# Kernel optimization log

Hardware: AMD Instinct MI355X
Metric: run time of the kernel (lower is better)

The kernel has to match this reference:

```python
import jax, jax.numpy as jnp
import numpy as np

B, S, E, H, FFN, NQ, DEPTH = 2, 2048, 1024, 16, 4096, 4, 2
DK = E // H
LN_EPS = 1e-5


def _layernorm(t, g, b):
    m = t.mean(-1, keepdims=True)
    v = ((t - m) ** 2).mean(-1, keepdims=True)
    return (t - m) / jnp.sqrt(v + LN_EPS) * g + b


def setup_inputs() -> dict:
    key = jax.random.key(0)
    ks = jax.random.split(key, 12)
    n = lambda i, shape, sc=1.0: (jax.random.normal(ks[i], shape, jnp.float32) * sc)
    return {
        "x": n(0, (B, S, E)),
        "wq": n(1, (E, E), 0.02),
        "wk": n(2, (E, E), 0.02),
        "wv": n(3, (E, E), 0.02),
        "wo": n(4, (E, E), 0.02),
        "w1": n(5, (E, FFN), 0.02),
        "b1": jnp.zeros((FFN,), jnp.float32),
        "w2": n(6, (FFN, E), 0.02),
        "b2": jnp.zeros((E,), jnp.float32),
        "qp_attn": n(7, (NQ, DEPTH)),
        "qp_ffn": n(8, (NQ, DEPTH)),
        "ln1_g": jnp.ones((E,), jnp.float32),
        "ln1_b": jnp.zeros((E,), jnp.float32),
        "ln2_g": jnp.ones((E,), jnp.float32),
        "ln2_b": jnp.zeros((E,), jnp.float32),
    }


def reference(x, wq, wk, wv, wo, w1, b1, w2, b2, qp_attn, qp_ffn,
              ln1_g, ln1_b, ln2_g, ln2_b):
    b, s, _ = x.shape
    # --- quantum attention ---
    q = (x @ wq).reshape(b, s, H, DK)
    k = (x @ wk).reshape(b, s, H, DK)
    v = (x @ wv).reshape(b, s, H, DK)
    scores = jnp.einsum('bqhd,bkhd->bhqk', q, k) / np.sqrt(DK).astype(np.float32)
    attn = jax.nn.softmax(scores, axis=-1)
    classical = jnp.einsum('bhqk,bkhd->bqhd', attn, v)  # (b, s, H, DK)
    # depth-2 RX-only circuit on |0..0>: <Z_0> = cos(sum_d params[0, d]);
    # data-independent scalar broadcast to the first NQ channels of each head
    c_attn = jnp.cos(qp_attn[0].sum())
    mixed = classical.at[..., :NQ].add(c_attn)
    attn_out = mixed.reshape(b, s, E) @ wo
    x1 = _layernorm(x + attn_out, ln1_g, ln1_b)  # dropout is identity in eval
    # --- quantum feed-forward ---
    h = x1 @ w1 + b1  # computed in the source but never consumed by the circuit
    # depth-2 RY-only circuit: <Z_0> = cos(sum_d params[0, d]) -- also data-free
    c_ffn = jnp.cos(qp_ffn[0].sum())
    qvec = jnp.zeros((FFN,), x.dtype).at[:NQ].set(c_ffn)
    ffn_out = jax.nn.relu(qvec) @ w2 + b2  # (E,), broadcast per token
    return _layernorm(x1 + ffn_out, ln2_g, ln2_b)
```

## Files before the change

kernel.cpp:

```cpp
#include <hip/hip_runtime.h>
#include <hip/hip_bf16.h>

typedef unsigned short u16;
using short8 = __attribute__((ext_vector_type(8))) short;
using f32x4  = __attribute__((ext_vector_type(4))) float;
using u32x2  = __attribute__((ext_vector_type(2))) unsigned;

#define S_  2048
#define E_  1024
#define H_  16
#define DK_ 64

#define GLP(p)  ((const __attribute__((address_space(1))) void*)(p))
#define LDSP(p) ((__attribute__((address_space(3))) void*)(p))

__device__ __forceinline__ float b2f(u16 u) {
  union { unsigned int i; float f; } v; v.i = ((unsigned int)u) << 16; return v.f;
}
__device__ __forceinline__ u16 f2b(float f) {
  union { float f; unsigned int i; } v; v.f = f;
  unsigned int r = v.i + 0x7fffu + ((v.i >> 16) & 1u);
  return (u16)(r >> 16);
}
__device__ __forceinline__ unsigned pk2(float a, float b) {
  __hip_bfloat162 h = __float22bfloat162_rn(make_float2(a, b));
  union { __hip_bfloat162 h; unsigned u; } c; c.h = h; return c.u;
}
__device__ __forceinline__ float fexp2(float x) {
#if __has_builtin(__builtin_amdgcn_exp2f)
  return __builtin_amdgcn_exp2f(x);
#else
  return exp2f(x);
#endif
}
__device__ __forceinline__ void plane32_swap(unsigned &dst, unsigned &src) {
#if __has_builtin(__builtin_amdgcn_permlane32_swap)
  u32x2 r = __builtin_amdgcn_permlane32_swap(dst, src, false, false);
  dst = r[0]; src = r[1];
#else
  asm volatile("v_permlane32_swap_b32 %0, %1" : "+v"(dst), "+v"(src));
#endif
}
__device__ __forceinline__ void plane16_swap(unsigned &dst, unsigned &src) {
#if __has_builtin(__builtin_amdgcn_permlane16_swap)
  u32x2 r = __builtin_amdgcn_permlane16_swap(dst, src, false, false);
  dst = r[0]; src = r[1];
#else
  asm volatile("v_permlane16_swap_b32 %0, %1" : "+v"(dst), "+v"(src));
#endif
}

__global__ __launch_bounds__(256) void prep_k(
    const float* __restrict__ x,
    const float* __restrict__ wq, const float* __restrict__ wk,
    const float* __restrict__ wv, const float* __restrict__ wo,
    const float* __restrict__ w2, const float* __restrict__ b2,
    const float* __restrict__ qpf,
    u16* __restrict__ xb, u16* __restrict__ wt, float* __restrict__ fv) {
  __shared__ u16 tile[64][65];
  int id = blockIdx.x, t = threadIdx.x;
  if (id < 2048) {
    size_t i = ((size_t)id * 256 + t) * 8;
    float4 a = *(const float4*)&x[i];
    float4 b = *(const float4*)&x[i + 4];
    uint4 o;
    o.x = pk2(a.x, a.y); o.y = pk2(a.z, a.w);
    o.z = pk2(b.x, b.y); o.w = pk2(b.z, b.w);
    *(uint4*)&xb[i] = o;
  } else if (id < 3072) {
    int i = id - 2048;
    int z = i >> 8; i &= 255;
    const float* src = (z == 0) ? wq : (z == 1) ? wk : (z == 2) ? wv : wo;
    u16* dst = wt + (size_t)z * E_ * E_;
    int k0 = (i & 15) * 64, n0 = (i >> 4) * 64;
    int rr = t >> 4, c4 = (t & 15) * 4;
    for (int p = 0; p < 4; p++) {
      int r = p * 16 + rr;
      float4 v = *(const float4*)&src[(size_t)(k0 + r) * E_ + n0 + c4];
      tile[r][c4] = f2b(v.x); tile[r][c4 + 1] = f2b(v.y);
      tile[r][c4 + 2] = f2b(v.z); tile[r][c4 + 3] = f2b(v.w);
    }
    __syncthreads();
    for (int p = 0; p < 4; p++) {
      int r = p * 16 + rr;
      ushort4 o;
      o.x = tile[c4][r]; o.y = tile[c4 + 1][r]; o.z = tile[c4 + 2][r]; o.w = tile[c4 + 3][r];
      *(ushort4*)&dst[(size_t)(n0 + r) * E_ + k0 + c4] = o;
    }
  } else {
    int e = (id - 3072) * 256 + t;
    float r = fmaxf(cosf(qpf[0] + qpf[1]), 0.f);
    fv[e] = b2[e] + r * (w2[0 * E_ + e] + w2[1 * E_ + e] + w2[2 * E_ + e] + w2[3 * E_ + e]);
  }
}

__device__ __forceinline__ void gemm_loop97(
    const u16* __restrict__ A, const u16* __restrict__ Bt,
    int m0, int n0, f32x4 acc[4][4], u16 (*As)[128][32], u16 (*Bs)[128][32]) {
  int t = threadIdx.x, lane = t & 63, w = t >> 6;
  int wm = w >> 1, wn = w & 1, l15 = lane & 15, quad = lane >> 4;
  int srow = lane >> 2, sch = (lane & 3) * 8;
  const u16 *ga[2], *gb[2];
#pragma unroll
  for (int p = 0; p < 2; p++) {
    int seg = w * 2 + p;
    ga[p] = A + (size_t)(m0 + seg * 16 + srow) * E_ + sch;
    gb[p] = Bt + (size_t)(n0 + seg * 16 + srow) * E_ + sch;
  }
#pragma unroll
  for (int p = 0; p < 2; p++) {
    int seg = w * 2 + p;
    __builtin_amdgcn_global_load_lds(GLP(ga[p]), LDSP(&As[0][seg * 16][0]), 16, 0, 0);
    __builtin_amdgcn_global_load_lds(GLP(gb[p]), LDSP(&Bs[0][seg * 16][0]), 16, 0, 0);
    ga[p] += 32; gb[p] += 32;
  }
  for (int i = 0; i < 32; i++) {
    __syncthreads();
    if (i + 1 < 32) {
      int nb = (i + 1) & 1;
#pragma unroll
      for (int p = 0; p < 2; p++) {
        int seg = w * 2 + p;
        __builtin_amdgcn_global_load_lds(GLP(ga[p]), LDSP(&As[nb][seg * 16][0]), 16, 0, 0);
        __builtin_amdgcn_global_load_lds(GLP(gb[p]), LDSP(&Bs[nb][seg * 16][0]), 16, 0, 0);
        ga[p] += 32; gb[p] += 32;
      }
    }
    int cb = i & 1;
    short8 af[4], bf[4];
#pragma unroll
    for (int ii = 0; ii < 4; ii++) af[ii] = *(const short8*)&As[cb][wm * 64 + ii * 16 + l15][quad * 8];
#pragma unroll
    for (int j = 0; j < 4; j++) bf[j] = *(const short8*)&Bs[cb][wn * 64 + j * 16 + l15][quad * 8];
#pragma unroll
    for (int ii = 0; ii < 4; ii++)
#pragma unroll
      for (int j = 0; j < 4; j++)
        acc[ii][j] = __builtin_amdgcn_mfma_f32_16x16x32_bf16(af[ii], bf[j], acc[ii][j], 0, 0, 0);
  }
}

__global__ __launch_bounds__(256) void qkv_gemm(
    const u16* __restrict__ xb, const u16* __restrict__ wt,
    u16* __restrict__ q, u16* __restrict__ k, u16* __restrict__ vt) {
  __shared__ __align__(16) u16 As[2][128][32];
  __shared__ __align__(16) u16 Bs[2][128][32];
  int bid = blockIdx.x + blockIdx.y * 8;
  int swz = (bid & 7) * 32 + (bid >> 3);
  int n0 = (swz & 7) * 128, m0 = (swz >> 3) * 128, z = blockIdx.z;
  const u16* Bt = wt + (size_t)z * E_ * E_;
  f32x4 acc[4][4];
  f32x4 zero = {0.f, 0.f, 0.f, 0.f};
  for (int i = 0; i < 4; i++)
    for (int j = 0; j < 4; j++) acc[i][j] = zero;
  gemm_loop97(xb, Bt, m0, n0, acc, As, Bs);
  int t = threadIdx.x, lane = t & 63, w = t >> 6;
  int wm = w >> 1, wn = w & 1, l15 = lane & 15, quad = lane >> 4;
  if (z < 2) {
    u16* out = (z == 0) ? q : k;
    float sc = (z == 0) ? 0.18033688f : 1.f;
#pragma unroll
    for (int i = 0; i < 4; i++)
#pragma unroll
      for (int j = 0; j < 4; j++) {
        int mm = m0 + wm * 64 + i * 16 + quad * 4;
        int nn = n0 + wn * 64 + j * 16 + l15;
#pragma unroll
        for (int rr = 0; rr < 4; rr++)
          out[(size_t)(mm + rr) * E_ + nn] = f2b(acc[i][j][rr] * sc);
      }
  } else {
#pragma unroll
    for (int i = 0; i < 4; i++)
#pragma unroll
      for (int j = 0; j < 4; j++) {
        int mm = m0 + wm * 64 + i * 16 + quad * 4;
        int nn = n0 + wn * 64 + j * 16 + l15;
        int b = mm >> 11, s = mm & (S_ - 1);
        size_t base = ((size_t)(b * H_ + (nn >> 6)) * DK_ + (nn & 63)) * S_ + s;
        ushort4 pk;
        pk.x = f2b(acc[i][j][0]); pk.y = f2b(acc[i][j][1]);
        pk.z = f2b(acc[i][j][2]); pk.w = f2b(acc[i][j][3]);
        *(ushort4*)&vt[base] = pk;
      }
  }
}

__global__ __launch_bounds__(256) void oproj_gemm(
    const u16* __restrict__ am, const u16* __restrict__ wot, float* __restrict__ proj) {
  __shared__ __align__(16) u16 As[2][128][32];
  __shared__ __align__(16) u16 Bs[2][128][32];
  int bid = blockIdx.x + blockIdx.y * 8;
  int swz = (bid & 7) * 32 + (bid >> 3);
  int n0 = (swz & 7) * 128, m0 = (swz >> 3) * 128;
  f32x4 acc[4][4];
  f32x4 zero = {0.f, 0.f, 0.f, 0.f};
  for (int i = 0; i < 4; i++)
    for (int j = 0; j < 4; j++) acc[i][j] = zero;
  gemm_loop97(am, wot, m0, n0, acc, As, Bs);
  int t = threadIdx.x, lane = t & 63, w = t >> 6;
  int wm = w >> 1, wn = w & 1, l15 = lane & 15, quad = lane >> 4;
#pragma unroll
  for (int i = 0; i < 4; i++)
#pragma unroll
    for (int j = 0; j < 4; j++) {
      int mm = m0 + wm * 64 + i * 16 + quad * 4;
      int nn = n0 + wn * 64 + j * 16 + l15;
#pragma unroll
      for (int rr = 0; rr < 4; rr++)
        proj[(size_t)(mm + rr) * E_ + nn] = acc[i][j][rr];
    }
}

__global__ __launch_bounds__(256, 4) void attn_kernel(
    const u16* __restrict__ q, const u16* __restrict__ kk,
    const u16* __restrict__ vt, const float* __restrict__ qpa,
    u16* __restrict__ outm) {
  __shared__ __align__(16) u16 KV[2][2][64][64];
  int bid = blockIdx.x + blockIdx.y * 32;
  int swz = (bid & 7) * 128 + (bid >> 3);
  int qt = swz & 31, bh = swz >> 5;
  int b = bh >> 4, h = bh & 15;
  int q0 = qt * 64;
  int t = threadIdx.x, lane = t & 63, w = t >> 6;
  int l15 = lane & 15, quad = lane >> 4;
  int qh = w >> 1, kh = w & 1;
  float c_attn = cosf(qpa[0] + qpa[1]);
  int r8 = lane >> 3, slot = lane & 7;
  size_t kbase = (size_t)(b * S_) * E_ + h * DK_;
  size_t vbase = (size_t)(b * H_ + h) * DK_ * S_;
  const u16 *kptr[2], *vptr[2];
#pragma unroll
  for (int p = 0; p < 2; p++) {
    int row = w * 16 + p * 8 + r8;
    int c = slot ^ (row & 7);
    kptr[p] = kk + kbase + (size_t)row * E_ + c * 8;
    vptr[p] = vt + vbase + (size_t)row * S_ + c * 8;
    __builtin_amdgcn_global_load_lds(GLP(kptr[p]), LDSP(&KV[0][0][w * 16 + p * 8][0]), 16, 0, 0);
    __builtin_amdgcn_global_load_lds(GLP(vptr[p]), LDSP(&KV[0][1][w * 16 + p * 8][0]), 16, 0, 0);
    kptr[p] += (size_t)64 * E_;
    vptr[p] += 64;
  }
  short8 bq[2][2];
#pragma unroll
  for (int nb = 0; nb < 2; nb++) {
    const u16* gq = q + (size_t)(b * S_ + q0 + qh * 32 + nb * 16 + l15) * E_ + h * DK_ + quad * 8;
    bq[nb][0] = *(const short8*)gq;
    bq[nb][1] = *(const short8*)(gq + 32);
  }
  short8 bones;
#pragma unroll
  for (int i = 0; i < 8; i++) bones[i] = (short)0x3F80;
  f32x4 O[2][4], Osum[2];
  f32x4 zero = {0.f, 0.f, 0.f, 0.f};
#pragma unroll
  for (int nb = 0; nb < 2; nb++) {
    Osum[nb] = zero;
#pragma unroll
    for (int j = 0; j < 4; j++) O[nb][j] = zero;
  }
  __syncthreads();
  for (int kt = 0; kt < S_ / 64; kt++) {
    if (kt) __syncthreads();
    if (kt + 1 < S_ / 64) {
      int nb2 = (kt + 1) & 1;
#pragma unroll
      for (int p = 0; p < 2; p++) {
        __builtin_amdgcn_global_load_lds(GLP(kptr[p]), LDSP(&KV[nb2][0][w * 16 + p * 8][0]), 16, 0, 0);
        __builtin_amdgcn_global_load_lds(GLP(vptr[p]), LDSP(&KV[nb2][1][w * 16 + p * 8][0]), 16, 0, 0);
        kptr[p] += (size_t)64 * E_;
        vptr[p] += 64;
      }
    }
    int cb = kt & 1;
    f32x4 sc[2][2];
    __builtin_amdgcn_s_setprio(1);
#pragma unroll
    for (int mb = 0; mb < 2; mb++) {
      int row = kh * 32 + mb * 16 + l15;
      int c0 = quad ^ (row & 7);
      short8 a0 = *(const short8*)&KV[cb][0][row][c0 * 8];
      short8 a1 = *(const short8*)&KV[cb][0][row][(c0 ^ 4) * 8];
#pragma unroll
      for (int nb = 0; nb < 2; nb++) {
        f32x4 z = __builtin_amdgcn_mfma_f32_16x16x32_bf16(a0, bq[nb][0], zero, 0, 0, 0);
        sc[mb][nb] = __builtin_amdgcn_mfma_f32_16x16x32_bf16(a1, bq[nb][1], z, 0, 0, 0);
      }
    }
    __builtin_amdgcn_s_setprio(0);
    short8 bv[4];
#pragma unroll
    for (int nd = 0; nd < 4; nd++) {
      int rv = nd * 16 + l15;
      int cv = (quad | (kh << 2)) ^ (rv & 7);
      bv[nd] = *(const short8*)&KV[cb][1][rv][cv * 8];
    }
    unsigned W[2][2][2];
#pragma unroll
    for (int mb = 0; mb < 2; mb++)
#pragma unroll
      for (int nb = 0; nb < 2; nb++) {
        float p0 = fexp2(sc[mb][nb][0]);
        float p1 = fexp2(sc[mb][nb][1]);
        float p2 = fexp2(sc[mb][nb][2]);
        float p3 = fexp2(sc[mb][nb][3]);
        W[mb][nb][0] = pk2(p0, p1);
        W[mb][nb][1] = pk2(p2, p3);
      }
    union AP { unsigned u[4]; short8 s; };
    AP ap[2];
#pragma unroll
    for (int nb = 0; nb < 2; nb++)
#pragma unroll
      for (int hh = 0; hh < 2; hh++) {
        unsigned a = W[0][nb][hh], bw = W[1][nb][hh];
        plane32_swap(bw, a);
        plane16_swap(a, bw);
        ap[nb].u[hh] = a; ap[nb].u[2 + hh] = bw;
      }
    __builtin_amdgcn_s_setprio(1);
#pragma unroll
    for (int nb = 0; nb < 2; nb++) {
#pragma unroll
      for (int nd = 0; nd < 4; nd++)
        O[nb][nd] = __builtin_amdgcn_mfma_f32_16x16x32_bf16(ap[nb].s, bv[nd], O[nb][nd], 0, 0, 0);
      Osum[nb] = __builtin_amdgcn_mfma_f32_16x16x32_bf16(ap[nb].s, bones, Osum[nb], 0, 0, 0);
    }
    __builtin_amdgcn_s_setprio(0);
  }
  float* red = (float*)KV;
  __syncthreads();
  if (kh) {
    float* dst = red + ((size_t)(qh * 64 + lane)) * 44;
#pragma unroll
    for (int nb = 0; nb < 2; nb++) {
#pragma unroll
      for (int nd = 0; nd < 4; nd++)
        *(f32x4*)&dst[nb * 16 + nd * 4] = O[nb][nd];
      *(f32x4*)&dst[32 + nb * 4] = Osum[nb];
    }
  }
  __syncthreads();
  if (!kh) {
    const float* src = red + ((size_t)(qh * 64 + lane)) * 44;
#pragma unroll
    for (int nb = 0; nb < 2; nb++) {
#pragma unroll
      for (int nd = 0; nd < 4; nd++) {
        f32x4 o2 = *(const f32x4*)&src[nb * 16 + nd * 4];
#pragma unroll
        for (int r = 0; r < 4; r++) O[nb][nd][r] += o2[r];
      }
      f32x4 s2 = *(const f32x4*)&src[32 + nb * 4];
#pragma unroll
      for (int r = 0; r < 4; r++) Osum[nb][r] += s2[r];
    }
#pragma unroll
    for (int nb = 0; nb < 2; nb++) {
      float inv[4];
#pragma unroll
      for (int r = 0; r < 4; r++) inv[r] = 1.f / Osum[nb][r];
#pragma unroll
      for (int nd = 0; nd < 4; nd++)
#pragma unroll
        for (int r = 0; r < 4; r++) {
          float val = O[nb][nd][r] * inv[r];
          int d = nd * 16 + l15;
          if (nd == 0 && l15 < 4) val += c_attn;
          int tok = b * S_ + q0 + qh * 32 + nb * 16 + quad * 4 + r;
          outm[(size_t)tok * E_ + h * DK_ + d] = f2b(val);
        }
    }
  }
}

__global__ __launch_bounds__(256) void ln_fused(
    const float* __restrict__ x, const float* __restrict__ proj, const float* __restrict__ fv,
    const float* __restrict__ g1, const float* __restrict__ bb1,
    const float* __restrict__ g2, const float* __restrict__ bb2,
    float* __restrict__ out) {
  __shared__ float sm[8];
  int tok = blockIdx.x, t = threadIdx.x;
  int e0 = t * 4;
  float4 xv = *(const float4*)&x[(size_t)tok * E_ + e0];
  float4 pv = *(const float4*)&proj[(size_t)tok * E_ + e0];
  float v0 = xv.x + pv.x, v1 = xv.y + pv.y;
  float v2 = xv.z + pv.z, v3 = xv.w + pv.w;
  float s = v0 + v1 + v2 + v3;
  float sq = v0 * v0 + v1 * v1 + v2 * v2 + v3 * v3;
  for (int m = 32; m >= 1; m >>= 1) { s += __shfl_xor(s, m, 64); sq += __shfl_xor(sq, m, 64); }
  int wid = t >> 6, lane = t & 63;
  if (lane == 0) { sm[wid] = s; sm[4 + wid] = sq; }
  __syncthreads();
  s = sm[0] + sm[1] + sm[2] + sm[3];
  sq = sm[4] + sm[5] + sm[6] + sm[7];
  float mean = s * (1.f / E_);
  float var = sq * (1.f / E_) - mean * mean;
  float rstd = rsqrtf(var + 1e-5f);
  float4 g1v = *(const float4*)&g1[e0];
  float4 b1v = *(const float4*)&bb1[e0];
  float4 fvv = *(const float4*)&fv[e0];
  float t0 = (v0 - mean) * rstd * g1v.x + b1v.x + fvv.x;
  float t1 = (v1 - mean) * rstd * g1v.y + b1v.y + fvv.y;
  float t2 = (v2 - mean) * rstd * g1v.z + b1v.z + fvv.z;
  float t3 = (v3 - mean) * rstd * g1v.w + b1v.w + fvv.w;
  float s2 = t0 + t1 + t2 + t3;
  float sq2 = t0 * t0 + t1 * t1 + t2 * t2 + t3 * t3;
  for (int m = 32; m >= 1; m >>= 1) { s2 += __shfl_xor(s2, m, 64); sq2 += __shfl_xor(sq2, m, 64); }
  __syncthreads();
  if (lane == 0) { sm[wid] = s2; sm[4 + wid] = sq2; }
  __syncthreads();
  s2 = sm[0] + sm[1] + sm[2] + sm[3];
  sq2 = sm[4] + sm[5] + sm[6] + sm[7];
  float mean2 = s2 * (1.f / E_);
  float var2 = sq2 * (1.f / E_) - mean2 * mean2;
  float rstd2 = rsqrtf(var2 + 1e-5f);
  float4 g2v = *(const float4*)&g2[e0];
  float4 b2v = *(const float4*)&bb2[e0];
  float4 ov;
  ov.x = (t0 - mean2) * rstd2 * g2v.x + b2v.x;
  ov.y = (t1 - mean2) * rstd2 * g2v.y + b2v.y;
  ov.z = (t2 - mean2) * rstd2 * g2v.z + b2v.z;
  ov.w = (t3 - mean2) * rstd2 * g2v.w + b2v.w;
  *(float4*)&out[(size_t)tok * E_ + e0] = ov;
}

extern "C" void kernel_launch(void* const* d_in, const int* in_sizes, int n_in,
                              void* d_out, int out_size, void* d_ws, size_t ws_size,
                              hipStream_t stream) {
  const float* x   = (const float*)d_in[0];
  const float* wq  = (const float*)d_in[1];
  const float* wk  = (const float*)d_in[2];
  const float* wv  = (const float*)d_in[3];
  const float* wo  = (const float*)d_in[4];
  const float* w2  = (const float*)d_in[7];
  const float* b2  = (const float*)d_in[8];
  const float* qpa = (const float*)d_in[9];
  const float* qpf = (const float*)d_in[10];
  const float* g1  = (const float*)d_in[11];
  const float* bb1 = (const float*)d_in[12];
  const float* g2  = (const float*)d_in[13];
  const float* bb2 = (const float*)d_in[14];

  char* ws = (char*)d_ws;
  u16* wt     = (u16*)ws;
  u16* q      = (u16*)(ws + (size_t)8  * 1048576);
  u16* k      = (u16*)(ws + (size_t)16 * 1048576);
  float* proj = (float*)(ws + (size_t)8 * 1048576);
  float* fv   = (float*)(ws + (size_t)24 * 1048576);
  u16* xb     = (u16*)d_out;
  u16* am     = (u16*)d_out;
  u16* vt     = (u16*)d_out + (size_t)4 * 1048576;
  float* outp = (float*)d_out;

  prep_k<<<dim3(3076), 256, 0, stream>>>(x, wq, wk, wv, wo, w2, b2, qpf, xb, wt, fv);
  qkv_gemm<<<dim3(8, 32, 3), 256, 0, stream>>>(xb, wt, q, k, vt);
  attn_kernel<<<dim3(32, 32), 256, 0, stream>>>(q, k, vt, qpa, am);
  oproj_gemm<<<dim3(8, 32), 256, 0, stream>>>(am, wt + (size_t)3 * E_ * E_, proj);
  ln_fused<<<dim3(4096), 256, 0, stream>>>(x, proj, fv, g1, bb1, g2, bb2, outp);
}
```

Before: 244.3 us.

## Software-pipeline attention loop so PV of previous tile overlaps QK of current

Restructures the attention K-loop so each iteration issues the QK^T MFMAs for the current key tile, then does exp/pack and the PV MFMAs for the previous tile, carrying scores and V fragments in registers across iterations. The last tile's PV runs in an epilogue after the loop. The aim is to let the exp and permute VALU work overlap with the independent score MFMAs and hide MFMA latency. In exchange it needs more live registers for the carried scores and V fragments, which may reduce occupancy.

```diff
diff --git a/kernel.cpp b/kernel.cpp
--- a/kernel.cpp
+++ b/kernel.cpp
@@ -259,6 +259,9 @@
 #pragma unroll
     for (int j = 0; j < 4; j++) O[nb][j] = zero;
   }
+  f32x4 scp[2][2];
+  short8 bvp[4];
+  union AP { unsigned u[4]; short8 s; };
   __syncthreads();
   for (int kt = 0; kt < S_ / 64; kt++) {
     if (kt) __syncthreads();
@@ -273,7 +276,7 @@
       }
     }
     int cb = kt & 1;
-    f32x4 sc[2][2];
+    f32x4 scc[2][2];
     __builtin_amdgcn_s_setprio(1);
 #pragma unroll
     for (int mb = 0; mb < 2; mb++) {
@@ -284,30 +287,67 @@
 #pragma unroll
       for (int nb = 0; nb < 2; nb++) {
         f32x4 z = __builtin_amdgcn_mfma_f32_16x16x32_bf16(a0, bq[nb][0], zero, 0, 0, 0);
-        sc[mb][nb] = __builtin_amdgcn_mfma_f32_16x16x32_bf16(a1, bq[nb][1], z, 0, 0, 0);
+        scc[mb][nb] = __builtin_amdgcn_mfma_f32_16x16x32_bf16(a1, bq[nb][1], z, 0, 0, 0);
       }
     }
     __builtin_amdgcn_s_setprio(0);
-    short8 bv[4];
+    if (kt) {
+      unsigned W[2][2][2];
+#pragma unroll
+      for (int mb = 0; mb < 2; mb++)
+#pragma unroll
+        for (int nb = 0; nb < 2; nb++) {
+          float p0 = fexp2(scp[mb][nb][0]);
+          float p1 = fexp2(scp[mb][nb][1]);
+          float p2 = fexp2(scp[mb][nb][2]);
+          float p3 = fexp2(scp[mb][nb][3]);
+          W[mb][nb][0] = pk2(p0, p1);
+          W[mb][nb][1] = pk2(p2, p3);
+        }
+      AP ap[2];
+#pragma unroll
+      for (int nb = 0; nb < 2; nb++)
+#pragma unroll
+        for (int hh = 0; hh < 2; hh++) {
+          unsigned a = W[0][nb][hh], bw = W[1][nb][hh];
+          plane32_swap(bw, a);
+          plane16_swap(a, bw);
+          ap[nb].u[hh] = a; ap[nb].u[2 + hh] = bw;
+        }
+      __builtin_amdgcn_s_setprio(1);
+#pragma unroll
+      for (int nb = 0; nb < 2; nb++) {
+#pragma unroll
+        for (int nd = 0; nd < 4; nd++)
+          O[nb][nd] = __builtin_amdgcn_mfma_f32_16x16x32_bf16(ap[nb].s, bvp[nd], O[nb][nd], 0, 0, 0);
+        Osum[nb] = __builtin_amdgcn_mfma_f32_16x16x32_bf16(ap[nb].s, bones, Osum[nb], 0, 0, 0);
+      }
+      __builtin_amdgcn_s_setprio(0);
+    }
 #pragma unroll
     for (int nd = 0; nd < 4; nd++) {
       int rv = nd * 16 + l15;
       int cv = (quad | (kh << 2)) ^ (rv & 7);
-      bv[nd] = *(const short8*)&KV[cb][1][rv][cv * 8];
-    }
+      bvp[nd] = *(const short8*)&KV[cb][1][rv][cv * 8];
+    }
+#pragma unroll
+    for (int mb = 0; mb < 2; mb++)
+#pragma unroll
+      for (int nb = 0; nb < 2; nb++) scp[mb][nb] = scc[mb][nb];
+  }
+  {
     unsigned W[2][2][2];
 #pragma unroll
     for (int mb = 0; mb < 2; mb++)
 #pragma unroll
       for (int nb = 0; nb < 2; nb++) {
-        float p0 = fexp2(sc[mb][nb][0]);
-        float p1 = fexp2(sc[mb][nb][1]);
-        float p2 = fexp2(sc[mb][nb][2]);
-        float p3 = fexp2(sc[mb][nb][3]);
+        float p0 = fexp2(scp[mb][nb][0]);
+        float p1 = fexp2(scp[mb][nb][1]);
+        float p2 = fexp2(scp[mb][nb][2]);
+        float p3 = fexp2(scp[mb][nb][3]);
         W[mb][nb][0] = pk2(p0, p1);
         W[mb][nb][1] = pk2(p2, p3);
       }
-    union AP { unsigned u[4]; short8 s; };
     AP ap[2];
 #pragma unroll
     for (int nb = 0; nb < 2; nb++)
@@ -318,15 +358,13 @@
         plane16_swap(a, bw);
         ap[nb].u[hh] = a; ap[nb].u[2 + hh] = bw;
       }
-    __builtin_amdgcn_s_setprio(1);
 #pragma unroll
     for (int nb = 0; nb < 2; nb++) {
 #pragma unroll
       for (int nd = 0; nd < 4; nd++)
-        O[nb][nd] = __builtin_amdgcn_mfma_f32_16x16x32_bf16(ap[nb].s, bv[nd], O[nb][nd], 0, 0, 0);
+        O[nb][nd] = __builtin_amdgcn_mfma_f32_16x16x32_bf16(ap[nb].s, bvp[nd], O[nb][nd], 0, 0, 0);
       Osum[nb] = __builtin_amdgcn_mfma_f32_16x16x32_bf16(ap[nb].s, bones, Osum[nb], 0, 0, 0);
     }
-    __builtin_amdgcn_s_setprio(0);
   }
   float* red = (float*)KV;
   __syncthreads();
```

New measurement: 245.5 us. No clear change (+0.5%).
